# Optimization experiments

Hardware: AMD Instinct MI355X
Metric: run time of the kernel (lower is better)

The kernel has to match this reference:

```python
import jax, jax.numpy as jnp
import numpy as np

# ---- module constants (kernel is hardcoded in scattering.__init__) ----
V_NODES = 2048
D_F = 128
J = 8              # filter-bank size (scaling + wavelets j=2..J)
L_LAYERS = 2       # scattering depth
R = 3.0
K = 1
DCOEF = (0.5, 0.5)
LAMB_MAX = 2.0
A = R * float(np.log(LAMB_MAX)) / (J - R + 1)  # kernel.a


def setup_inputs() -> dict:
    key = jax.random.key(0)
    kW, kf = jax.random.split(key)
    Araw = jax.random.uniform(kW, (V_NODES, V_NODES), dtype=jnp.float32)
    # symmetric adjacency with row sums ~0.9 (<1): distinct eigenvalues, wavelets active
    W = (Araw + Araw.T) * (0.9 / V_NODES)
    f = jax.random.normal(kf, (V_NODES, D_F), dtype=jnp.float32)
    return {"W": W, "f": f}


def _g_hat(x):
    # vectorized kernel.g_hat: sum_k d[k] cos(2*pi*k*(x/A + 0.5)) on (-A, 0], else 0
    d = jnp.asarray(DCOEF, dtype=x.dtype)
    ks = jnp.arange(K + 1, dtype=x.dtype)
    val = jnp.sum(d * jnp.cos(2.0 * jnp.pi * ks * (x[..., None] / A + 0.5)), axis=-1)
    return jnp.where((x > -A) & (x <= 0.0), val, 0.0)


def _filter_responses(E):
    # E: [V] eigenvalues -> [J, V] responses (row 0 = scaling, rows 1.. = wavelets j=2..J)
    js = jnp.arange(2, J + 1, dtype=E.dtype)                      # [J-1]
    wav = _g_hat(jnp.log(E)[None, :] - A * (js[:, None] - 1.0) / R)  # [J-1, V]
    d = jnp.asarray(DCOEF, dtype=E.dtype)
    s = (R / 2.0) * jnp.sum(d ** 2) + (R / 2.0) * d[0] ** 2 - jnp.sum(wav ** 2, axis=0)
    scal = jnp.sqrt(jnp.maximum(s, 0.0))                          # kernel.scaling
    return jnp.concatenate([scal[None, :], wav], axis=0)          # [J, V]


def reference(W, f):
    # compute_spectrum: NOTE source builds L = D (degrees only, no -W) then normalizes
    deg = W.sum(1)                                   # [V]
    dhalf = 1.0 / jnp.sqrt(jnp.maximum(1.0, deg))    # diag of D^{-1/2} with clamp
    Lmat = jnp.diag(deg) * dhalf[:, None] * dhalf[None, :]
    E, Vv = jnp.linalg.eigh(Lmat)
    E = jnp.abs(E)
    lam = _filter_responses(E)                       # [J, V]
    # filtering matrices g_j = V diag(lam_j) V^T, all j at once
    g = jnp.einsum('ai,ji,bi->jab', Vv, lam, Vv)     # [J, V, V]
    parts = [f.mean(0)]                              # S starts as f.mean(0)
    U = f[None]                                      # [1, V, d_f]
    for _ in range(L_LAYERS):
        # loop order in source: for f_ in U: for g_j in g -> index (u, j), u-major
        U = jnp.abs(jnp.einsum('jvw,uwd->ujvd', g, U)).reshape(-1, V_NODES, D_F)
        parts.append(U.mean(1).reshape(-1))          # concat of per-branch means
    return jnp.concatenate(parts)                    # [d_f*(1+J+J^2)]
```

## Files before the change

### kernel.cpp

```cpp
#include <hip/hip_runtime.h>
#include <math.h>

#define V 2048
#define DF 128
#define NK 73
#define NSLICE 32
#define A_F 0.34657359027997264f
#define TWO_PI_F 6.283185307179586f

__global__ __launch_bounds__(256) void k_filters(const float* __restrict__ W,
                                                 float* __restrict__ c) {
    __shared__ float red[4];
    const int v = blockIdx.x;
    const int tid = threadIdx.x;
    const float4* row = (const float4*)(W + (size_t)v * V);
    float4 a = row[tid];
    float4 b = row[tid + 256];
    float s = ((a.x + a.y) + (a.z + a.w)) + ((b.x + b.y) + (b.z + b.w));
    #pragma unroll
    for (int off = 32; off > 0; off >>= 1) s += __shfl_down(s, off, 64);
    if ((tid & 63) == 0) red[tid >> 6] = s;
    __syncthreads();
    if (tid == 0) {
        float deg = (red[0] + red[1]) + (red[2] + red[3]);
        float e = fabsf(deg / fmaxf(1.0f, deg));
        float x = logf(e);
        float sumsq = 0.0f, wv[7];
        #pragma unroll
        for (int j = 2; j <= 8; ++j) {
            float t = x - A_F * (float)(j - 1) * (1.0f / 3.0f);
            float val = 0.0f;
            if (t > -A_F && t <= 0.0f)
                val = 0.5f + 0.5f * cosf(TWO_PI_F * (t / A_F + 0.5f));
            wv[j - 2] = val;
            sumsq += val * val;
        }
        c[v] = sqrtf(fmaxf(1.125f - sumsq, 0.0f));
        #pragma unroll
        for (int j = 0; j < 7; ++j) c[(j + 1) * V + v] = wv[j];
    }
}

__global__ __launch_bounds__(128) void k_scatter(const float* __restrict__ f,
                                                 const float* __restrict__ c,
                                                 float* __restrict__ part) {
    const int k = blockIdx.x;
    const int sl = blockIdx.y;
    const int d = threadIdx.x;
    const int v0 = sl * (V / NSLICE);
    const int v1 = v0 + (V / NSLICE);
    float acc = 0.0f;
    if (k == 0) {
        #pragma unroll 16
        for (int v = v0; v < v1; ++v)
            acc += f[(size_t)v * DF + d];
    } else if (k <= 8) {
        const float* cj = c + (k - 1) * V;
        #pragma unroll 16
        for (int v = v0; v < v1; ++v)
            acc += cj[v] * fabsf(f[(size_t)v * DF + d]);
    } else {
        const float* c1 = c + ((k - 9) >> 3) * V;
        const float* c2 = c + ((k - 9) & 7) * V;
        #pragma unroll 16
        for (int v = v0; v < v1; ++v)
            acc += c1[v] * c2[v] * fabsf(f[(size_t)v * DF + d]);
    }
    part[((size_t)sl * NK + k) * DF + d] = acc;
}

__global__ __launch_bounds__(256) void k_reduce(const float* __restrict__ part,
                                               float* __restrict__ out) {
    const int i = blockIdx.x * 256 + threadIdx.x;
    if (i < NK * DF) {
        float s = 0.0f;
        #pragma unroll
        for (int sl = 0; sl < NSLICE; ++sl) s += part[(size_t)sl * NK * DF + i];
        out[i] = s * (1.0f / (float)V);
    }
}

extern "C" void kernel_launch(void* const* d_in, const int* in_sizes, int n_in,
                              void* d_out, int out_size, void* d_ws, size_t ws_size,
                              hipStream_t stream) {
    const float* W = (const float*)d_in[0];
    const float* f = (const float*)d_in[1];
    float* out = (float*)d_out;

    float* c    = (float*)d_ws;
    float* part = c + 8 * V;

    k_filters<<<V, 256, 0, stream>>>(W, c);
    k_scatter<<<dim3(NK, NSLICE), DF, 0, stream>>>(f, c, part);
    k_reduce<<<(NK * DF + 255) / 256, 256, 0, stream>>>(part, out);
}
```

Measured before the change: 72.32 us.

## Fuse filter computation and scattering accumulation into one per-chunk kernel

Merges the degree/filter-response kernel with the scattering accumulation. Each 512-thread block now handles 8 nodes: it sums their W rows, computes the 8 filter responses in shared memory, and accumulates all 73 outputs per feature column, with the products split across four thread groups. A second kernel reduces the 256 per-block partials. This drops one launch and the round-trip of the filter coefficients through global memory, and avoids re-reading f for every output k. In exchange the partial buffer is much larger (256×73×128 floats) and the final reduction has more data to read.

After: 70.85 us. -2.0%, faster.

```diff
diff --git a/kernel.cpp b/kernel.cpp
--- a/kernel.cpp
+++ b/kernel.cpp
@@ -4,79 +4,147 @@
 #define V 2048
 #define DF 128
 #define NK 73
-#define NSLICE 32
+#define CH 8
+#define G1 (V / CH)
+#define OUT_N (NK * DF)
 #define A_F 0.34657359027997264f
 #define TWO_PI_F 6.283185307179586f
 
-__global__ __launch_bounds__(256) void k_filters(const float* __restrict__ W,
-                                                 float* __restrict__ c) {
-    __shared__ float red[4];
-    const int v = blockIdx.x;
-    const int tid = threadIdx.x;
-    const float4* row = (const float4*)(W + (size_t)v * V);
-    float4 a = row[tid];
-    float4 b = row[tid + 256];
-    float s = ((a.x + a.y) + (a.z + a.w)) + ((b.x + b.y) + (b.z + b.w));
+__global__ __launch_bounds__(512) void k_fused(const float* __restrict__ W,
+                                               const float* __restrict__ f,
+                                               float* __restrict__ partial) {
+    const int b = blockIdx.x;
+    const int t = threadIdx.x;
+    const int wave = t >> 6, lane = t & 63;
+    const int v0 = b * CH;
+    const int d = t & 127;
+
+    __shared__ float wps[8][CH];
+    __shared__ __align__(16) float wmat[CH][8];
+
+    float fvv[CH];
     #pragma unroll
-    for (int off = 32; off > 0; off >>= 1) s += __shfl_down(s, off, 64);
-    if ((tid & 63) == 0) red[tid >> 6] = s;
+    for (int r = 0; r < CH; ++r)
+        fvv[r] = f[(v0 + r) * DF + d];
+
+    float p[CH];
+    #pragma unroll
+    for (int r = 0; r < CH; ++r) {
+        float4 x = ((const float4*)(W + (size_t)(v0 + r) * V))[t];
+        p[r] = (x.x + x.y) + (x.z + x.w);
+    }
+    #pragma unroll
+    for (int off = 32; off > 0; off >>= 1) {
+        #pragma unroll
+        for (int r = 0; r < CH; ++r) p[r] += __shfl_xor(p[r], off, 64);
+    }
+    if (lane == 0) {
+        #pragma unroll
+        for (int r = 0; r < CH; ++r) wps[wave][r] = p[r];
+    }
     __syncthreads();
-    if (tid == 0) {
-        float deg = (red[0] + red[1]) + (red[2] + red[3]);
-        float e = fabsf(deg / fmaxf(1.0f, deg));
-        float x = logf(e);
-        float sumsq = 0.0f, wv[7];
+
+    if (t < 64) {
+        const int r = t >> 3, jj = t & 7;
+        if (jj > 0) {
+            float deg = 0.0f;
+            #pragma unroll
+            for (int wv = 0; wv < 8; ++wv) deg += wps[wv][r];
+            float e = fabsf(deg / fmaxf(1.0f, deg));
+            float x = logf(e);
+            float tt = x - A_F * (float)jj * (1.0f / 3.0f);
+            float val = 0.0f;
+            if (tt > -A_F && tt <= 0.0f)
+                val = 0.5f + 0.5f * cosf(TWO_PI_F * (tt / A_F + 0.5f));
+            wmat[r][jj] = val;
+        }
+    }
+    __syncthreads();
+    if (t < CH) {
+        float sumsq = 0.0f;
         #pragma unroll
-        for (int j = 2; j <= 8; ++j) {
-            float t = x - A_F * (float)(j - 1) * (1.0f / 3.0f);
-            float val = 0.0f;
-            if (t > -A_F && t <= 0.0f)
-                val = 0.5f + 0.5f * cosf(TWO_PI_F * (t / A_F + 0.5f));
-            wv[j - 2] = val;
-            sumsq += val * val;
+        for (int jj = 1; jj < 8; ++jj) sumsq += wmat[t][jj] * wmat[t][jj];
+        wmat[t][0] = sqrtf(fmaxf(1.125f - sumsq, 0.0f));
+    }
+    __syncthreads();
+
+    const int rep = t >> 7;
+    float acc[19];
+    #pragma unroll
+    for (int i = 0; i < 19; ++i) acc[i] = 0.0f;
+
+    #pragma unroll
+    for (int r = 0; r < CH; ++r) {
+        const float fv = fvv[r];
+        const float af = fabsf(fv);
+        const float4 wa = *(const float4*)&wmat[r][0];
+        const float4 wb = *(const float4*)&wmat[r][4];
+        const float w0 = wa.x, w1 = wa.y, w2 = wa.z, w3 = wa.w;
+        const float w4 = wb.x, w5 = wb.y, w6 = wb.z, w7 = wb.w;
+        if (rep == 0) {
+            acc[0] += fv;
+            acc[1] += w0 * af; acc[2] += w1 * af; acc[3] += w2 * af; acc[4] += w3 * af;
+            acc[5] += w4 * af; acc[6] += w5 * af; acc[7] += w6 * af; acc[8] += w7 * af;
+            const float c0 = w0 * af;
+            acc[9]  += c0 * w0; acc[10] += c0 * w1; acc[11] += c0 * w2; acc[12] += c0 * w3;
+            acc[13] += c0 * w4; acc[14] += c0 * w5; acc[15] += c0 * w6; acc[16] += c0 * w7;
+            const float c1 = w1 * af;
+            acc[17] += c1 * w0; acc[18] += c1 * w1;
+        } else if (rep == 1) {
+            const float c1 = w1 * af;
+            acc[0] += c1 * w2; acc[1] += c1 * w3; acc[2] += c1 * w4;
+            acc[3] += c1 * w5; acc[4] += c1 * w6; acc[5] += c1 * w7;
+            const float c2 = w2 * af;
+            acc[6]  += c2 * w0; acc[7]  += c2 * w1; acc[8]  += c2 * w2; acc[9]  += c2 * w3;
+            acc[10] += c2 * w4; acc[11] += c2 * w5; acc[12] += c2 * w6; acc[13] += c2 * w7;
+            const float c3 = w3 * af;
+            acc[14] += c3 * w0; acc[15] += c3 * w1; acc[16] += c3 * w2; acc[17] += c3 * w3;
+        } else if (rep == 2) {
+            const float c3 = w3 * af;
+            acc[0] += c3 * w4; acc[1] += c3 * w5; acc[2] += c3 * w6; acc[3] += c3 * w7;
+            const float c4 = w4 * af;
+            acc[4]  += c4 * w0; acc[5]  += c4 * w1; acc[6]  += c4 * w2; acc[7]  += c4 * w3;
+            acc[8]  += c4 * w4; acc[9]  += c4 * w5; acc[10] += c4 * w6; acc[11] += c4 * w7;
+            const float c5 = w5 * af;
+            acc[12] += c5 * w0; acc[13] += c5 * w1; acc[14] += c5 * w2;
+            acc[15] += c5 * w3; acc[16] += c5 * w4; acc[17] += c5 * w5;
+        } else {
+            const float c5 = w5 * af;
+            acc[0] += c5 * w6; acc[1] += c5 * w7;
+            const float c6 = w6 * af;
+            acc[2] += c6 * w0; acc[3] += c6 * w1; acc[4] += c6 * w2; acc[5] += c6 * w3;
+            acc[6] += c6 * w4; acc[7] += c6 * w5; acc[8] += c6 * w6; acc[9] += c6 * w7;
+            const float c7 = w7 * af;
+            acc[10] += c7 * w0; acc[11] += c7 * w1; acc[12] += c7 * w2; acc[13] += c7 * w3;
+            acc[14] += c7 * w4; acc[15] += c7 * w5; acc[16] += c7 * w6; acc[17] += c7 * w7;
         }
-        c[v] = sqrtf(fmaxf(1.125f - sumsq, 0.0f));
-        #pragma unroll
-        for (int j = 0; j < 7; ++j) c[(j + 1) * V + v] = wv[j];
     }
+
+    const int kbase = (rep == 0) ? 0 : 1 + rep * 18;
+    const int nacc  = (rep == 0) ? 19 : 18;
+    float* pb = partial + (size_t)b * OUT_N + d;
+    #pragma unroll
+    for (int i = 0; i < 19; ++i)
+        if (i < nacc) pb[(kbase + i) * DF] = acc[i];
 }
 
-__global__ __launch_bounds__(128) void k_scatter(const float* __restrict__ f,
-                                                 const float* __restrict__ c,
-                                                 float* __restrict__ part) {
-    const int k = blockIdx.x;
-    const int sl = blockIdx.y;
-    const int d = threadIdx.x;
-    const int v0 = sl * (V / NSLICE);
-    const int v1 = v0 + (V / NSLICE);
-    float acc = 0.0f;
-    if (k == 0) {
-        #pragma unroll 16
-        for (int v = v0; v < v1; ++v)
-            acc += f[(size_t)v * DF + d];
-    } else if (k <= 8) {
-        const float* cj = c + (k - 1) * V;
-        #pragma unroll 16
-        for (int v = v0; v < v1; ++v)
-            acc += cj[v] * fabsf(f[(size_t)v * DF + d]);
-    } else {
-        const float* c1 = c + ((k - 9) >> 3) * V;
-        const float* c2 = c + ((k - 9) & 7) * V;
-        #pragma unroll 16
-        for (int v = v0; v < v1; ++v)
-            acc += c1[v] * c2[v] * fabsf(f[(size_t)v * DF + d]);
-    }
-    part[((size_t)sl * NK + k) * DF + d] = acc;
-}
-
-__global__ __launch_bounds__(256) void k_reduce(const float* __restrict__ part,
-                                               float* __restrict__ out) {
-    const int i = blockIdx.x * 256 + threadIdx.x;
-    if (i < NK * DF) {
-        float s = 0.0f;
+__global__ __launch_bounds__(256) void k_out(const float* __restrict__ partial,
+                                             float* __restrict__ out) {
+    const int t = threadIdx.x;
+    const int o = t & 31, g = t >> 5;
+    const int i0 = blockIdx.x * 32;
+    float s = 0.0f;
+    #pragma unroll
+    for (int kk = 0; kk < 32; ++kk)
+        s += partial[(size_t)(g * 32 + kk) * OUT_N + i0 + o];
+    __shared__ float red[8][32];
+    red[g][o] = s;
+    __syncthreads();
+    if (t < 32) {
+        float tot = 0.0f;
         #pragma unroll
-        for (int sl = 0; sl < NSLICE; ++sl) s += part[(size_t)sl * NK * DF + i];
-        out[i] = s * (1.0f / (float)V);
+        for (int gg = 0; gg < 8; ++gg) tot += red[gg][t];
+        out[i0 + t] = tot * (1.0f / (float)V);
     }
 }
 
@@ -87,10 +155,8 @@
     const float* f = (const float*)d_in[1];
     float* out = (float*)d_out;
 
-    float* c    = (float*)d_ws;
-    float* part = c + 8 * V;
+    float* partial = (float*)d_ws;
 
-    k_filters<<<V, 256, 0, stream>>>(W, c);
-    k_scatter<<<dim3(NK, NSLICE), DF, 0, stream>>>(f, c, part);
-    k_reduce<<<(NK * DF + 255) / 256, 256, 0, stream>>>(part, out);
+    k_fused<<<G1, 512, 0, stream>>>(W, f, partial);
+    k_out<<<OUT_N / 32, 256, 0, stream>>>(partial, out);
 }
```
